# Optimization experiments

Hardware: AMD Instinct MI355X
Metric: run time of the kernel (lower is better)

The kernel has to match this reference:

```python
import jax, jax.numpy as jnp
import numpy as np

B = 512          # batch == number of memories
S = 8            # num_attention_splits
U = 512          # num_units = sum(num_units_regions)
D = 32           # dim_attention_unit
G = 8            # num_attention_groups
MASK_P = 0.1
DIM_IN = 4096
DAG = 2048       # dim_attention_global


def setup_inputs() -> dict:
    key = jax.random.key(0)
    ks = jax.random.split(key, 8)
    # xavier-normal-ish scales for the unit-wise linears
    s1 = (2.0 / (DIM_IN // S + DAG // S)) ** 0.5
    s2 = (2.0 / (DAG // S + U * D // S)) ** 0.5
    return {
        "x": jax.random.normal(ks[0], (B, DIM_IN), jnp.float32),
        "mem_attention": jax.random.normal(ks[1], (B, U, D), jnp.float32),
        "mem_outputs": jax.random.normal(ks[2], (B, U, D), jnp.float32),
        "rand_u": jax.random.uniform(ks[3], (B, B, U), jnp.float32),
        "w1": jax.random.normal(ks[4], (S, DIM_IN // S, DAG // S), jnp.float32) * s1,
        "b1": jnp.zeros((S, DAG // S), jnp.float32),
        "w2": jax.random.normal(ks[5], (S, DAG // S, U * D // S), jnp.float32) * s2,
        "b2": jnp.zeros((S, U * D // S), jnp.float32),
        "temperature": jnp.ones((U,), jnp.float32),
    }


def reference(x, mem_attention, mem_outputs, rand_u, w1, b1, w2, b2, temperature):
    # attentions(): split input, two unit-wise linears
    xs = x.reshape(B, S, DIM_IN // S)                        # [B,S,I/S]
    ga = jnp.einsum("bsi,sio->bso", xs, w1) + b1             # [B,S,DAG/S]
    att = jnp.einsum("bso,soj->bsj", ga, w2) + b2            # [B,S,U*D/S]
    att = att.reshape(B, U, D)                               # [B,U,D]
    ga_flat = ga.reshape(B, DAG)                             # [B,DAG]

    # per-unit pairwise scores: (att_b . mem_att_m) per unit  -> [B,M,U]
    weights = jnp.einsum("bud,mud->bmu", att, mem_attention)
    weights = weights * temperature                          # broadcast over U

    neg_inf = jnp.float32(-jnp.inf)
    weights = jnp.where(rand_u < MASK_P, neg_inf, weights)   # random mask
    eye = jnp.eye(B, dtype=bool)[:, :, None]                 # self-exclusion
    weights = jnp.where(eye, neg_inf, weights)

    # group-wise softmax over the memory axis
    w = weights.reshape(B, B // G, G, U)
    w = jax.nn.softmax(w, axis=1)
    w = w.reshape(B, B, U) / 8.0

    # weighted reduction over memories (avoids [B,B,U,D] intermediate)
    outputs = jnp.einsum("bmu,mud->bud", w, mem_outputs)     # [B,U,D]
    return att, ga_flat, w, outputs
```

## Files before the change

### kernel.cpp

```cpp
#include <hip/hip_runtime.h>
#include <math.h>

#define NEGBIG (-1e30f)
#define GLB_PTR(x) ((const __attribute__((address_space(1))) void*)(x))
#define LDS_PTR(x) ((__attribute__((address_space(3))) void*)(x))

typedef __bf16 bf16x8 __attribute__((ext_vector_type(8)));
typedef float  f32x4  __attribute__((ext_vector_type(4)));


__global__ __launch_bounds__(256) void gemm_split(
    const float* __restrict__ A, int lda, int Ksz,
    const float* __restrict__ Bw, int NS,
    const float* __restrict__ bias,
    float* __restrict__ C, int ldc)
{
  const int n0 = blockIdx.x * 64;
  const int b0 = blockIdx.y * 64;
  const int s  = n0 / NS;
  const float* Bp = Bw + (size_t)s * Ksz * NS;
  const int nloc0 = n0 - s * NS;
  const int acol0 = s * Ksz;

  __shared__ float As[16][64];
  __shared__ float Bs[16][64];

  const int t  = threadIdx.x;
  const int tb = t & 15, tn = t >> 4;
  float acc[4][4] = {};

  for (int k0 = 0; k0 < Ksz; k0 += 16) {
    {
      int r = t & 63, g = t >> 6;
      float4 v = *reinterpret_cast<const float4*>(
          A + (size_t)(b0 + r) * lda + acol0 + k0 + 4 * g);
      As[4*g+0][r] = v.x; As[4*g+1][r] = v.y; As[4*g+2][r] = v.z; As[4*g+3][r] = v.w;
    }
    {
      int kk = t >> 4, n4 = t & 15;
      float4 v = *reinterpret_cast<const float4*>(
          Bp + (size_t)(k0 + kk) * NS + nloc0 + 4 * n4);
      *reinterpret_cast<float4*>(&Bs[kk][4*n4]) = v;
    }
    __syncthreads();
#pragma unroll
    for (int k = 0; k < 16; ++k) {
      float4 a4 = *reinterpret_cast<const float4*>(&As[k][4*tb]);
      float4 b4 = *reinterpret_cast<const float4*>(&Bs[k][4*tn]);
      float av[4] = {a4.x, a4.y, a4.z, a4.w};
      float bv[4] = {b4.x, b4.y, b4.z, b4.w};
#pragma unroll
      for (int i = 0; i < 4; ++i)
#pragma unroll
        for (int j = 0; j < 4; ++j)
          acc[i][j] = fmaf(av[i], bv[j], acc[i][j]);
    }
    __syncthreads();
  }
#pragma unroll
  for (int i = 0; i < 4; ++i) {
    int row = b0 + 4*tb + i;
    int col = n0 + 4*tn;
    float4 o;
    o.x = acc[i][0] + bias[col + 0];
    o.y = acc[i][1] + bias[col + 1];
    o.z = acc[i][2] + bias[col + 2];
    o.w = acc[i][3] + bias[col + 3];
    *reinterpret_cast<float4*>(C + (size_t)row * ldc + col) = o;
  }
}

__global__ __launch_bounds__(256) void scores_mfma_v2(
    const float* __restrict__ att,
    const float* __restrict__ ma,
    const float* __restrict__ rnd,
    const float* __restrict__ temp,
    float* __restrict__ wout,
    float* __restrict__ stats)
{
  __shared__ float MaL[2048 * 4];
  __shared__ float tr[256 * 17];
  const int b0 = blockIdx.x * 16;
  const int u0 = blockIdx.y * 16;
  const int t  = threadIdx.x;
  const int w  = t >> 6, l = t & 63;
  const int lm = l & 15, kb = l >> 4;
  const int bl = t >> 4, ml = t & 15;
  const int gb = b0 + bl;

  float tvf[16];
#pragma unroll
  for (int q = 0; q < 4; ++q) {
    float4 tq = *reinterpret_cast<const float4*>(temp + u0 + 4 * q);
    tvf[4*q+0] = tq.x; tvf[4*q+1] = tq.y; tvf[4*q+2] = tq.z; tvf[4*q+3] = tq.w;
  }

  bf16x8 Ahi[4], Alo[4];
#pragma unroll
  for (int q = 0; q < 4; ++q) {
    const float* ap = att + (size_t)(b0 + lm) * 16384
                    + (size_t)(u0 + 4 * w + q) * 32 + kb * 8;
    float4 a0 = *reinterpret_cast<const float4*>(ap);
    float4 a1 = *reinterpret_cast<const float4*>(ap + 4);
    float af[8] = {a0.x, a0.y, a0.z, a0.w, a1.x, a1.y, a1.z, a1.w};
#pragma unroll
    for (int j = 0; j < 8; ++j) {
      __bf16 h = (__bf16)af[j];
      Ahi[q][j] = h;
      Alo[q][j] = (__bf16)(af[j] - (float)h);
    }
  }

  int off[8];
#pragma unroll
  for (int k = 0; k < 8; ++k) {
    int s = k * 256 + t;
    int mm = s >> 7, uu = (s >> 3) & 15, d4s = s & 7;
    off[k] = mm * 16384 + (u0 + uu) * 32 + ((d4s ^ (mm & 7)) << 2);
  }

  float Ls[16];
#pragma unroll
  for (int u = 0; u < 16; ++u) Ls[u] = 0.f;

  const float* rb = rnd  + (size_t)gb * 262144 + u0;
  float*       wb = wout + (size_t)gb * 262144 + u0;

#pragma unroll
  for (int k = 0; k < 8; ++k)
    __builtin_amdgcn_global_load_lds(GLB_PTR(ma + (size_t)off[k]),
                                     LDS_PTR(&MaL[(k * 256 + w * 64) * 4]), 16, 0, 0);

#pragma unroll 1
  for (int c = 0; c < 32; ++c) {
    const int m0 = c * 16;
    __syncthreads();

    float4 rv[4];
#pragma unroll
    for (int q = 0; q < 4; ++q)
      rv[q] = *reinterpret_cast<const float4*>(rb + (size_t)(m0 + ml) * 512 + 4 * q);

#pragma unroll
    for (int q = 0; q < 4; ++q) {
      const int uq = 4 * w + q;
      const int s0 = (lm << 7) + (uq << 3) + ((2 * kb)     ^ (lm & 7));
      const int s1 = (lm << 7) + (uq << 3) + ((2 * kb + 1) ^ (lm & 7));
      float4 g0 = *reinterpret_cast<const float4*>(&MaL[s0 * 4]);
      float4 g1 = *reinterpret_cast<const float4*>(&MaL[s1 * 4]);
      float bf[8] = {g0.x, g0.y, g0.z, g0.w, g1.x, g1.y, g1.z, g1.w};
      bf16x8 Bhi, Blo;
#pragma unroll
      for (int j = 0; j < 8; ++j) {
        __bf16 h = (__bf16)bf[j];
        Bhi[j] = h;
        Blo[j] = (__bf16)(bf[j] - (float)h);
      }
      f32x4 acc = {0.f, 0.f, 0.f, 0.f};
      acc = __builtin_amdgcn_mfma_f32_16x16x32_bf16(Ahi[q], Blo, acc, 0, 0, 0);
      acc = __builtin_amdgcn_mfma_f32_16x16x32_bf16(Alo[q], Bhi, acc, 0, 0, 0);
      acc = __builtin_amdgcn_mfma_f32_16x16x32_bf16(Ahi[q], Bhi, acc, 0, 0, 0);
#pragma unroll
      for (int i = 0; i < 4; ++i)
        tr[((kb * 4 + i) * 16 + lm) * 17 + uq] = acc[i];
    }
    __syncthreads();

    if (c < 31) {
#pragma unroll
      for (int k = 0; k < 8; ++k)
        __builtin_amdgcn_global_load_lds(
            GLB_PTR(ma + (size_t)off[k] + (size_t)(m0 + 16) * 16384),
            LDS_PTR(&MaL[(k * 256 + w * 64) * 4]), 16, 0, 0);
    }

    const int gm = m0 + ml;
    const bool dg = (gm == gb);
    const float* trow = &tr[(bl * 16 + ml) * 17];
    float* wp = wb + (size_t)gm * 512;
#pragma unroll
    for (int q = 0; q < 4; ++q) {
      float rr[4] = {rv[q].x, rv[q].y, rv[q].z, rv[q].w};
      float sv[4];
#pragma unroll
      for (int e = 0; e < 4; ++e) {
        const int u = 4 * q + e;
        float p;
        if ((rr[e] < 0.1f) | dg) p = 0.f;
        else                     p = __expf(trow[u] * tvf[u]);
        sv[e] = p;
        Ls[u] += p;
      }
      *reinterpret_cast<float4*>(wp + 4 * q) =
          make_float4(sv[0], sv[1], sv[2], sv[3]);
    }
  }

  float tot[16];
#pragma unroll
  for (int u = 0; u < 16; ++u)
    tot[u] = Ls[u] + __shfl_xor(Ls[u], 8, 64);
  if (ml < 8) {
#pragma unroll
    for (int u = 0; u < 16; ++u)
      stats[((size_t)gb * 512 + u0 + u) * 32 + ml] = 1.0f / (8.0f * tot[u]);
  }
}

__global__ __launch_bounds__(256) void emit_outputs_v3(
    const float* __restrict__ mo,
    float* __restrict__ w,
    float* __restrict__ outs)
{
  __shared__ float MoL[8 * 16 * 32];
  __shared__ float E[8 * 16 * 17];
  const int u0 = blockIdx.x * 16;
  const int b0 = blockIdx.y * 16;
  const int t  = threadIdx.x;
  const int ab = t >> 4, am = (t >> 1) & 7, uh = t & 1;
  const int pu = t >> 4, bq = (t >> 2) & 3, dh = t & 3;

  float Sreg[8];
  {
    const float* cb = outs + ((size_t)(b0 + ab) * 512 + u0 + uh * 8) * 32;
#pragma unroll
    for (int j = 0; j < 8; ++j) Sreg[j] = cb[j * 32 + am];
  }

  float4 acc[4][2];
#pragma unroll
  for (int i = 0; i < 4; ++i) {
    acc[i][0] = make_float4(0.f, 0.f, 0.f, 0.f);
    acc[i][1] = make_float4(0.f, 0.f, 0.f, 0.f);
  }

  float* wbase = w + (size_t)(b0 + ab) * 262144 + u0 + uh * 8;

  const float* msrc0;  const float* msrc1;  const float* msrc2;  const float* msrc3;
  int loff0, loff1, loff2, loff3;
  {
    int P, mm, uu, dq;
    P = t;          mm = P >> 7; uu = (P >> 3) & 15; dq = P & 7;
    msrc0 = mo + (size_t)mm * 16384 + (size_t)(u0 + uu) * 32 + (dq ^ (uu & 7)) * 4;
    loff0 = P * 4;
    P = 256 + t;    mm = P >> 7; uu = (P >> 3) & 15; dq = P & 7;
    msrc1 = mo + (size_t)mm * 16384 + (size_t)(u0 + uu) * 32 + (dq ^ (uu & 7)) * 4;
    loff1 = P * 4;
    P = 512 + t;    mm = P >> 7; uu = (P >> 3) & 15; dq = P & 7;
    msrc2 = mo + (size_t)mm * 16384 + (size_t)(u0 + uu) * 32 + (dq ^ (uu & 7)) * 4;
    loff2 = P * 4;
    P = 768 + t;    mm = P >> 7; uu = (P >> 3) & 15; dq = P & 7;
    msrc3 = mo + (size_t)mm * 16384 + (size_t)(u0 + uu) * 32 + (dq ^ (uu & 7)) * 4;
    loff3 = P * 4;
  }

  float4 wpre0, wpre1, smo0, smo1, smo2, smo3;
  {
    const float* wp = wbase + (size_t)am * 512;
    wpre0 = *reinterpret_cast<const float4*>(wp);
    wpre1 = *reinterpret_cast<const float4*>(wp + 4);
    smo0 = *reinterpret_cast<const float4*>(msrc0);
    smo1 = *reinterpret_cast<const float4*>(msrc1);
    smo2 = *reinterpret_cast<const float4*>(msrc2);
    smo3 = *reinterpret_cast<const float4*>(msrc3);
  }

#pragma unroll 1
  for (int c = 0; c < 64; ++c) {
    const int mc = c * 8;
    if (c) __syncthreads();

    {
      float* wp = wbase + (size_t)(mc + am) * 512;
      float s0[4] = {wpre0.x, wpre0.y, wpre0.z, wpre0.w};
      float s1[4] = {wpre1.x, wpre1.y, wpre1.z, wpre1.w};
#pragma unroll
      for (int e2 = 0; e2 < 4; ++e2) {
        float v = s0[e2] * Sreg[e2];
        s0[e2] = v;
        E[(am * 16 + uh * 8 + e2) * 17 + ab] = v;
      }
#pragma unroll
      for (int e2 = 0; e2 < 4; ++e2) {
        float v = s1[e2] * Sreg[4 + e2];
        s1[e2] = v;
        E[(am * 16 + uh * 8 + 4 + e2) * 17 + ab] = v;
      }
      *reinterpret_cast<float4*>(wp)     = make_float4(s0[0], s0[1], s0[2], s0[3]);
      *reinterpret_cast<float4*>(wp + 4) = make_float4(s1[0], s1[1], s1[2], s1[3]);
    }
    *reinterpret_cast<float4*>(&MoL[loff0]) = smo0;
    *reinterpret_cast<float4*>(&MoL[loff1]) = smo1;
    *reinterpret_cast<float4*>(&MoL[loff2]) = smo2;
    *reinterpret_cast<float4*>(&MoL[loff3]) = smo3;
    __syncthreads();

    if (c < 63) {
      const float* wp = wbase + (size_t)(mc + 8 + am) * 512;
      wpre0 = *reinterpret_cast<const float4*>(wp);
      wpre1 = *reinterpret_cast<const float4*>(wp + 4);
      const size_t moff = (size_t)(mc + 8) * 16384;
      smo0 = *reinterpret_cast<const float4*>(msrc0 + moff);
      smo1 = *reinterpret_cast<const float4*>(msrc1 + moff);
      smo2 = *reinterpret_cast<const float4*>(msrc2 + moff);
      smo3 = *reinterpret_cast<const float4*>(msrc3 + moff);
    }

#pragma unroll
    for (int m = 0; m < 8; ++m) {
      float4 ef = *reinterpret_cast<const float4*>(&E[(m * 16 + pu) * 17 + 4 * bq]);
      float4 v0 = *reinterpret_cast<const float4*>(
          &MoL[(m * 16 + pu) * 32 + (((2 * dh) ^ (pu & 7)) * 4)]);
      float4 v1 = *reinterpret_cast<const float4*>(
          &MoL[(m * 16 + pu) * 32 + (((2 * dh + 1) ^ (pu & 7)) * 4)]);
      float es[4] = {ef.x, ef.y, ef.z, ef.w};
#pragma unroll
      for (int i = 0; i < 4; ++i) {
        acc[i][0].x = fmaf(es[i], v0.x, acc[i][0].x);
        acc[i][0].y = fmaf(es[i], v0.y, acc[i][0].y);
        acc[i][0].z = fmaf(es[i], v0.z, acc[i][0].z);
        acc[i][0].w = fmaf(es[i], v0.w, acc[i][0].w);
        acc[i][1].x = fmaf(es[i], v1.x, acc[i][1].x);
        acc[i][1].y = fmaf(es[i], v1.y, acc[i][1].y);
        acc[i][1].z = fmaf(es[i], v1.z, acc[i][1].z);
        acc[i][1].w = fmaf(es[i], v1.w, acc[i][1].w);
      }
    }
  }

#pragma unroll
  for (int i = 0; i < 4; ++i) {
    float* dst = outs + ((size_t)(b0 + 4 * bq + i) * 512 + u0 + pu) * 32 + 8 * dh;
    *reinterpret_cast<float4*>(dst)     = acc[i][0];
    *reinterpret_cast<float4*>(dst + 4) = acc[i][1];
  }
}

extern "C" void kernel_launch(void* const* d_in, const int* in_sizes, int n_in,
                              void* d_out, int out_size, void* d_ws, size_t ws_size,
                              hipStream_t stream) {
  const float* x    = (const float*)d_in[0];
  const float* ma   = (const float*)d_in[1];
  const float* mo   = (const float*)d_in[2];
  const float* rnd  = (const float*)d_in[3];
  const float* w1   = (const float*)d_in[4];
  const float* b1   = (const float*)d_in[5];
  const float* w2   = (const float*)d_in[6];
  const float* b2   = (const float*)d_in[7];
  const float* temp = (const float*)d_in[8];

  float* out  = (float*)d_out;
  float* att  = out;
  float* ga   = out + 8388608;
  float* wbuf = out + 9437184;
  float* outs = out + 143654912;

  gemm_split<<<dim3(32, 8), 256, 0, stream>>>(x, 4096, 512, w1, 256, b1, ga, 2048);
  gemm_split<<<dim3(256, 8), 256, 0, stream>>>(ga, 2048, 256, w2, 2048, b2, att, 16384);
  scores_mfma_v2<<<dim3(32, 32), 256, 0, stream>>>(att, ma, rnd, temp, wbuf, outs);
  emit_outputs_v3<<<dim3(32, 32), 256, 0, stream>>>(mo, wbuf, outs);
}
```

Baseline: 906.4 us.

## Consume MFMA accumulators directly in scores kernel and swizzle block order

The scores kernel drops the LDS transpose buffer and applies masking and exp directly on MFMA accumulator registers, with each lane handling 4 batch rows × 4 units. Random-mask reads and weight writes are remapped to match the accumulator layout. A 1D grid with a block-id permutation changes which (b,u) tiles run concurrently, aiming for better cache locality of memory tiles. Each store is now a 16-byte chunk per lane per row rather than 64 contiguous bytes, which may reduce coalescing of the large rand and weight traffic.

```diff
diff --git a/kernel.cpp b/kernel.cpp
--- a/kernel.cpp
+++ b/kernel.cpp
@@ -70,7 +70,7 @@
   }
 }
 
-__global__ __launch_bounds__(256) void scores_mfma_v2(
+__global__ __launch_bounds__(256) void scores_mfma_v4(
     const float* __restrict__ att,
     const float* __restrict__ ma,
     const float* __restrict__ rnd,
@@ -79,21 +79,17 @@
     float* __restrict__ stats)
 {
   __shared__ float MaL[2048 * 4];
-  __shared__ float tr[256 * 17];
-  const int b0 = blockIdx.x * 16;
-  const int u0 = blockIdx.y * 16;
-  const int t  = threadIdx.x;
-  const int w  = t >> 6, l = t & 63;
-  const int lm = l & 15, kb = l >> 4;
-  const int bl = t >> 4, ml = t & 15;
-  const int gb = b0 + bl;
-
-  float tvf[16];
-#pragma unroll
-  for (int q = 0; q < 4; ++q) {
-    float4 tq = *reinterpret_cast<const float4*>(temp + u0 + 4 * q);
-    tvf[4*q+0] = tq.x; tvf[4*q+1] = tq.y; tvf[4*q+2] = tq.z; tvf[4*q+3] = tq.w;
-  }
+  const int bid = blockIdx.x;
+  const int id  = ((bid & 7) << 7) | (bid >> 3);
+  const int u0  = (id >> 5) * 16;
+  const int b0  = (id & 31) * 16;
+  const int t   = threadIdx.x;
+  const int w   = t >> 6, l = t & 63;
+  const int lm  = l & 15, kb = l >> 4;
+
+  float tv[4];
+#pragma unroll
+  for (int q = 0; q < 4; ++q) tv[q] = temp[u0 + 4 * w + q];
 
   bf16x8 Ahi[4], Alo[4];
 #pragma unroll
@@ -119,12 +115,16 @@
     off[k] = mm * 16384 + (u0 + uu) * 32 + ((d4s ^ (mm & 7)) << 2);
   }
 
-  float Ls[16];
-#pragma unroll
-  for (int u = 0; u < 16; ++u) Ls[u] = 0.f;
-
-  const float* rb = rnd  + (size_t)gb * 262144 + u0;
-  float*       wb = wout + (size_t)gb * 262144 + u0;
+  float Ls[4][4];
+#pragma unroll
+  for (int i = 0; i < 4; ++i)
+#pragma unroll
+    for (int q = 0; q < 4; ++q) Ls[i][q] = 0.f;
+
+  const float* rbl = rnd  + (size_t)(b0 + kb * 4) * 262144
+                   + (size_t)lm * 512 + u0 + 4 * w;
+  float*       wbl = wout + (size_t)(b0 + kb * 4) * 262144
+                   + (size_t)lm * 512 + u0 + 4 * w;
 
 #pragma unroll
   for (int k = 0; k < 8; ++k)
@@ -138,9 +138,11 @@
 
     float4 rv[4];
 #pragma unroll
-    for (int q = 0; q < 4; ++q)
-      rv[q] = *reinterpret_cast<const float4*>(rb + (size_t)(m0 + ml) * 512 + 4 * q);
-
+    for (int i = 0; i < 4; ++i)
+      rv[i] = *reinterpret_cast<const float4*>(rbl + (size_t)i * 262144
+                                               + (size_t)m0 * 512);
+
+    f32x4 acc[4];
 #pragma unroll
     for (int q = 0; q < 4; ++q) {
       const int uq = 4 * w + q;
@@ -156,13 +158,11 @@
         Bhi[j] = h;
         Blo[j] = (__bf16)(bf[j] - (float)h);
       }
-      f32x4 acc = {0.f, 0.f, 0.f, 0.f};
-      acc = __builtin_amdgcn_mfma_f32_16x16x32_bf16(Ahi[q], Blo, acc, 0, 0, 0);
-      acc = __builtin_amdgcn_mfma_f32_16x16x32_bf16(Alo[q], Bhi, acc, 0, 0, 0);
-      acc = __builtin_amdgcn_mfma_f32_16x16x32_bf16(Ahi[q], Bhi, acc, 0, 0, 0);
-#pragma unroll
-      for (int i = 0; i < 4; ++i)
-        tr[((kb * 4 + i) * 16 + lm) * 17 + uq] = acc[i];
+      f32x4 a = {0.f, 0.f, 0.f, 0.f};
+      a = __builtin_amdgcn_mfma_f32_16x16x32_bf16(Ahi[q], Blo, a, 0, 0, 0);
+      a = __builtin_amdgcn_mfma_f32_16x16x32_bf16(Alo[q], Bhi, a, 0, 0, 0);
+      a = __builtin_amdgcn_mfma_f32_16x16x32_bf16(Ahi[q], Bhi, a, 0, 0, 0);
+      acc[q] = a;
     }
     __syncthreads();
 
@@ -174,36 +174,38 @@
             LDS_PTR(&MaL[(k * 256 + w * 64) * 4]), 16, 0, 0);
     }
 
-    const int gm = m0 + ml;
-    const bool dg = (gm == gb);
-    const float* trow = &tr[(bl * 16 + ml) * 17];
-    float* wp = wb + (size_t)gm * 512;
-#pragma unroll
-    for (int q = 0; q < 4; ++q) {
-      float rr[4] = {rv[q].x, rv[q].y, rv[q].z, rv[q].w};
-      float sv[4];
-#pragma unroll
-      for (int e = 0; e < 4; ++e) {
-        const int u = 4 * q + e;
+    const int gm = m0 + lm;
+#pragma unroll
+    for (int i = 0; i < 4; ++i) {
+      const int gb = b0 + kb * 4 + i;
+      const bool dg = (gm == gb);
+      float rr[4] = {rv[i].x, rv[i].y, rv[i].z, rv[i].w};
+      float pv[4];
+#pragma unroll
+      for (int q = 0; q < 4; ++q) {
         float p;
-        if ((rr[e] < 0.1f) | dg) p = 0.f;
-        else                     p = __expf(trow[u] * tvf[u]);
-        sv[e] = p;
-        Ls[u] += p;
-      }
-      *reinterpret_cast<float4*>(wp + 4 * q) =
-          make_float4(sv[0], sv[1], sv[2], sv[3]);
-    }
-  }
-
-  float tot[16];
-#pragma unroll
-  for (int u = 0; u < 16; ++u)
-    tot[u] = Ls[u] + __shfl_xor(Ls[u], 8, 64);
-  if (ml < 8) {
-#pragma unroll
-    for (int u = 0; u < 16; ++u)
-      stats[((size_t)gb * 512 + u0 + u) * 32 + ml] = 1.0f / (8.0f * tot[u]);
+        if ((rr[q] < 0.1f) | dg) p = 0.f;
+        else                     p = __expf(acc[q][i] * tv[q]);
+        pv[q] = p;
+        Ls[i][q] += p;
+      }
+      *reinterpret_cast<float4*>(wbl + (size_t)i * 262144 + (size_t)m0 * 512) =
+          make_float4(pv[0], pv[1], pv[2], pv[3]);
+    }
+  }
+
+#pragma unroll
+  for (int i = 0; i < 4; ++i)
+#pragma unroll
+    for (int q = 0; q < 4; ++q)
+      Ls[i][q] += __shfl_xor(Ls[i][q], 8, 64);
+  if (lm < 8) {
+#pragma unroll
+    for (int i = 0; i < 4; ++i)
+#pragma unroll
+      for (int q = 0; q < 4; ++q)
+        stats[((size_t)(b0 + kb * 4 + i) * 512 + u0 + 4 * w + q) * 32 + lm] =
+            1.0f / (8.0f * Ls[i][q]);
   }
 }
 
@@ -357,6 +359,6 @@
 
   gemm_split<<<dim3(32, 8), 256, 0, stream>>>(x, 4096, 512, w1, 256, b1, ga, 2048);
   gemm_split<<<dim3(256, 8), 256, 0, stream>>>(ga, 2048, 256, w2, 2048, b2, att, 16384);
-  scores_mfma_v2<<<dim3(32, 32), 256, 0, stream>>>(att, ma, rnd, temp, wbuf, outs);
+  scores_mfma_v4<<<dim3(1024), 256, 0, stream>>>(att, ma, rnd, temp, wbuf, outs);
   emit_outputs_v3<<<dim3(32, 32), 256, 0, stream>>>(mo, wbuf, outs);
 }
```

After: 958.9 us. 5.8% more time.

## Remap softmax epilogue thread mapping, prefetch mask values, swizzle transpose buffer

Applied to the files above, without the earlier changes.

The epilogue of the scores kernel is remapped so each thread owns one unit and loops over 16 memories, instead of owning one memory and 16 units. The random-mask values for the next chunk are now prefetched into registers one iteration ahead, overlapping their load latency with the MFMA work. The transpose buffer gets an XOR swizzle to avoid LDS bank conflicts under the new access pattern. Per-group partial sums now live directly in per-thread registers, so the cross-lane shuffle is gone. The cost is that global reads and writes of rand_u and the weights become scalar strided accesses (stride 512 floats per thread) rather than float4 rows, and more registers are in use.

```diff
diff --git a/kernel.cpp b/kernel.cpp
--- a/kernel.cpp
+++ b/kernel.cpp
@@ -70,7 +70,7 @@
   }
 }
 
-__global__ __launch_bounds__(256) void scores_mfma_v2(
+__global__ __launch_bounds__(256) void scores_mfma_v5(
     const float* __restrict__ att,
     const float* __restrict__ ma,
     const float* __restrict__ rnd,
@@ -85,15 +85,10 @@
   const int t  = threadIdx.x;
   const int w  = t >> 6, l = t & 63;
   const int lm = l & 15, kb = l >> 4;
-  const int bl = t >> 4, ml = t & 15;
-  const int gb = b0 + bl;
-
-  float tvf[16];
-#pragma unroll
-  for (int q = 0; q < 4; ++q) {
-    float4 tq = *reinterpret_cast<const float4*>(temp + u0 + 4 * q);
-    tvf[4*q+0] = tq.x; tvf[4*q+1] = tq.y; tvf[4*q+2] = tq.z; tvf[4*q+3] = tq.w;
-  }
+  const int eu = t & 15, eb = t >> 4;
+  const int gbe = b0 + eb;
+
+  const float tmp = temp[u0 + eu];
 
   bf16x8 Ahi[4], Alo[4];
 #pragma unroll
@@ -119,27 +114,25 @@
     off[k] = mm * 16384 + (u0 + uu) * 32 + ((d4s ^ (mm & 7)) << 2);
   }
 
-  float Ls[16];
-#pragma unroll
-  for (int u = 0; u < 16; ++u) Ls[u] = 0.f;
-
-  const float* rb = rnd  + (size_t)gb * 262144 + u0;
-  float*       wb = wout + (size_t)gb * 262144 + u0;
+  float Ls[8];
+#pragma unroll
+  for (int g = 0; g < 8; ++g) Ls[g] = 0.f;
+
+  const float* rbase = rnd  + (size_t)gbe * 262144 + u0 + eu;
+  float*       wbase = wout + (size_t)gbe * 262144 + u0 + eu;
 
 #pragma unroll
   for (int k = 0; k < 8; ++k)
     __builtin_amdgcn_global_load_lds(GLB_PTR(ma + (size_t)off[k]),
                                      LDS_PTR(&MaL[(k * 256 + w * 64) * 4]), 16, 0, 0);
+  float rc[16], rn[16];
+#pragma unroll
+  for (int j = 0; j < 16; ++j) rc[j] = rbase[(size_t)j * 512];
 
 #pragma unroll 1
   for (int c = 0; c < 32; ++c) {
     const int m0 = c * 16;
     __syncthreads();
-
-    float4 rv[4];
-#pragma unroll
-    for (int q = 0; q < 4; ++q)
-      rv[q] = *reinterpret_cast<const float4*>(rb + (size_t)(m0 + ml) * 512 + 4 * q);
 
 #pragma unroll
     for (int q = 0; q < 4; ++q) {
@@ -156,13 +149,15 @@
         Bhi[j] = h;
         Blo[j] = (__bf16)(bf[j] - (float)h);
       }
-      f32x4 acc = {0.f, 0.f, 0.f, 0.f};
-      acc = __builtin_amdgcn_mfma_f32_16x16x32_bf16(Ahi[q], Blo, acc, 0, 0, 0);
-      acc = __builtin_amdgcn_mfma_f32_16x16x32_bf16(Alo[q], Bhi, acc, 0, 0, 0);
-      acc = __builtin_amdgcn_mfma_f32_16x16x32_bf16(Ahi[q], Bhi, acc, 0, 0, 0);
-#pragma unroll
-      for (int i = 0; i < 4; ++i)
-        tr[((kb * 4 + i) * 16 + lm) * 17 + uq] = acc[i];
+      f32x4 a = {0.f, 0.f, 0.f, 0.f};
+      a = __builtin_amdgcn_mfma_f32_16x16x32_bf16(Ahi[q], Blo, a, 0, 0, 0);
+      a = __builtin_amdgcn_mfma_f32_16x16x32_bf16(Alo[q], Bhi, a, 0, 0, 0);
+      a = __builtin_amdgcn_mfma_f32_16x16x32_bf16(Ahi[q], Bhi, a, 0, 0, 0);
+#pragma unroll
+      for (int i = 0; i < 4; ++i) {
+        const int row = (kb * 4 + i) * 16 + lm;
+        tr[row * 17 + (uq ^ ((row >> 6) << 2))] = a[i];
+      }
     }
     __syncthreads();
 
@@ -172,38 +167,30 @@
         __builtin_amdgcn_global_load_lds(
             GLB_PTR(ma + (size_t)off[k] + (size_t)(m0 + 16) * 16384),
             LDS_PTR(&MaL[(k * 256 + w * 64) * 4]), 16, 0, 0);
-    }
-
-    const int gm = m0 + ml;
-    const bool dg = (gm == gb);
-    const float* trow = &tr[(bl * 16 + ml) * 17];
-    float* wp = wb + (size_t)gm * 512;
-#pragma unroll
-    for (int q = 0; q < 4; ++q) {
-      float rr[4] = {rv[q].x, rv[q].y, rv[q].z, rv[q].w};
-      float sv[4];
-#pragma unroll
-      for (int e = 0; e < 4; ++e) {
-        const int u = 4 * q + e;
-        float p;
-        if ((rr[e] < 0.1f) | dg) p = 0.f;
-        else                     p = __expf(trow[u] * tvf[u]);
-        sv[e] = p;
-        Ls[u] += p;
-      }
-      *reinterpret_cast<float4*>(wp + 4 * q) =
-          make_float4(sv[0], sv[1], sv[2], sv[3]);
-    }
-  }
-
-  float tot[16];
-#pragma unroll
-  for (int u = 0; u < 16; ++u)
-    tot[u] = Ls[u] + __shfl_xor(Ls[u], 8, 64);
-  if (ml < 8) {
-#pragma unroll
-    for (int u = 0; u < 16; ++u)
-      stats[((size_t)gb * 512 + u0 + u) * 32 + ml] = 1.0f / (8.0f * tot[u]);
+#pragma unroll
+      for (int j = 0; j < 16; ++j)
+        rn[j] = rbase[(size_t)(m0 + 16 + j) * 512];
+    }
+
+    const int swz = (eb >> 2) << 2;
+    const float* trow = &tr[(eb * 16) * 17 + (eu ^ swz)];
+#pragma unroll
+    for (int j = 0; j < 16; ++j) {
+      const int gm = m0 + j;
+      float p;
+      if ((rc[j] < 0.1f) | (gm == gbe)) p = 0.f;
+      else                              p = __expf(trow[j * 17] * tmp);
+      wbase[(size_t)gm * 512] = p;
+      Ls[j & 7] += p;
+    }
+#pragma unroll
+    for (int j = 0; j < 16; ++j) rc[j] = rn[j];
+  }
+
+  {
+    float* cell = stats + ((size_t)gbe * 512 + u0 + eu) * 32;
+#pragma unroll
+    for (int g = 0; g < 8; ++g) cell[g] = 1.0f / (8.0f * Ls[g]);
   }
 }
 
@@ -357,6 +344,6 @@
 
   gemm_split<<<dim3(32, 8), 256, 0, stream>>>(x, 4096, 512, w1, 256, b1, ga, 2048);
   gemm_split<<<dim3(256, 8), 256, 0, stream>>>(ga, 2048, 256, w2, 2048, b2, att, 16384);
-  scores_mfma_v2<<<dim3(32, 32), 256, 0, stream>>>(att, ma, rnd, temp, wbuf, outs);
+  scores_mfma_v5<<<dim3(32, 32), 256, 0, stream>>>(att, ma, rnd, temp, wbuf, outs);
   emit_outputs_v3<<<dim3(32, 32), 256, 0, stream>>>(mo, wbuf, outs);
 }
```

After: 822.5 us. 1.1x faster.
